# Performance work log

Measured on AMD Instinct MI355X. Metric: run time of the kernel, lower is better.

## Reference

```python
import jax, jax.numpy as jnp
import numpy as np

D = 1024      # d_model
ED = 2048     # d_inner
K = 4         # d_conv
N = 16        # d_state
R = 64        # dt_rank
E = 8         # num_experts
TOPK = 2      # num_experts_per_tok
FF = 2048     # mlp_size
EPS = 1e-6
B, L = 1, 2048


def setup_inputs() -> dict:
    key = jax.random.key(0)
    ks = jax.random.split(key, 12)
    def nrm(k, shape, scale=0.02):
        return jax.random.normal(k, shape, jnp.float32) * scale
    return {
        "x": jax.random.normal(ks[0], (B, L, D), jnp.float32),
        "rms1_w": jnp.ones((D,), jnp.float32),
        "rms2_w": jnp.ones((D,), jnp.float32),
        "W_in": nrm(ks[1], (2 * ED, D)),
        "conv_w": nrm(ks[2], (ED, 1, K), 0.1),
        "conv_b": jnp.zeros((ED,), jnp.float32),
        "W_xproj": nrm(ks[3], (R + 2 * N, ED)),
        "W_dt": nrm(ks[4], (ED, R), 0.1),
        "b_dt": jnp.full((ED,), -4.6, jnp.float32),  # softplus(-4.6) ~ 0.01 init dt
        "A_log": jnp.log(jnp.tile(jnp.arange(1, N + 1, dtype=jnp.float32), (ED, 1))),  # S4D-real init
        "D_skip": jnp.ones((ED,), jnp.float32),
        "W_out": nrm(ks[5], (D, ED)),
        "W_router": nrm(ks[6], (E, D)),
        "gate_w": nrm(ks[7], (E, FF, D)),
        "up_w": nrm(ks[8], (E, FF, D)),
        "down_w": nrm(ks[9], (E, D, FF)),
    }


def rmsnorm(x, w):
    return x * jax.lax.rsqrt(jnp.mean(x * x, -1, keepdims=True) + EPS) * w


def mamba(x, W_in, conv_w, conv_b, W_xproj, W_dt, b_dt, A_log, D_skip, W_out):
    Bb, Ll, _ = x.shape
    xm, z = jnp.split(x @ W_in.T, 2, axis=-1)                 # [B,L,ED] each
    # depthwise causal conv over time
    xc = jax.lax.conv_general_dilated(xm.transpose(0, 2, 1), conv_w, (1,), [(K - 1, 0)],
                                      feature_group_count=ED)  # [B,ED,L]
    xc = jax.nn.silu((xc + conv_b[None, :, None]).transpose(0, 2, 1))  # [B,L,ED]
    dt, Bm, Cm = jnp.split(xc @ W_xproj.T, [R, R + N], axis=-1)        # [B,L,R],[B,L,N],[B,L,N]
    delta = jax.nn.softplus(dt @ W_dt.T + b_dt)                        # [B,L,ED]
    A = -jnp.exp(A_log)                                                # [ED,N]
    dA = jnp.exp(delta[..., None] * A)                                 # [B,L,ED,N]
    dBx = delta[..., None] * Bm[:, :, None, :] * xc[..., None]         # [B,L,ED,N]

    def step(h, t):
        dA_t, dBx_t, C_t = t
        h = dA_t * h + dBx_t
        return h, jnp.einsum("ben,bn->be", h, C_t)

    h0 = jnp.zeros((Bb, ED, N), x.dtype)
    _, ys = jax.lax.scan(step, h0, (dA.transpose(1, 0, 2, 3), dBx.transpose(1, 0, 2, 3), Cm.transpose(1, 0, 2)))
    y = ys.transpose(1, 0, 2) + D_skip * xc
    y = y * jax.nn.silu(z)
    return y @ W_out.T


def moe(x2d, W_router, gate_w, up_w, down_w):
    logits = x2d @ W_router.T                                  # [T,E]
    probs = jax.nn.softmax(logits.astype(jnp.float32), -1)
    topw, sel = jax.lax.top_k(probs, TOPK)                     # NOTE: no renormalization (faithful)
    topw = topw.astype(x2d.dtype)
    wmat = jnp.sum(jax.nn.one_hot(sel, E, dtype=x2d.dtype) * topw[..., None], axis=1)  # [T,E]
    g = jnp.einsum("td,efd->tef", x2d, gate_w)
    u = jnp.einsum("td,efd->tef", x2d, up_w)
    h = jax.nn.silu(g) * u
    ye = jnp.einsum("tef,edf->ted", h, down_w)
    out = jnp.einsum("ted,te->td", ye, wmat)
    return out, logits


def reference(x, rms1_w, rms2_w, W_in, conv_w, conv_b, W_xproj, W_dt, b_dt, A_log,
              D_skip, W_out, W_router, gate_w, up_w, down_w):
    Bb, Ll, Dd = x.shape
    res = x
    h = rmsnorm(x, rms1_w)
    h = mamba(h, W_in, conv_w, conv_b, W_xproj, W_dt, b_dt, A_log, D_skip, W_out)
    x = res + h
    res = x
    h = rmsnorm(x, rms2_w)
    mo, logits = moe(h.reshape(-1, Dd), W_router, gate_w, up_w, down_w)
    x = res + mo.reshape(Bb, Ll, Dd)
    return (x, logits)
```

## Files before the change

kernel.cpp:

```cpp
#include <hip/hip_runtime.h>
#include <math.h>

typedef unsigned short u16;
typedef unsigned int   u32;
typedef __attribute__((ext_vector_type(8))) short bf16x8;
typedef __attribute__((ext_vector_type(4))) float f32x4;

constexpr int Tn=2048, Dm=1024, EDc=2048, Ns=16, Rr=64, NEx=8, FFc=2048;
constexpr int SCH=32, SNCH=Tn/SCH;
constexpr int MAXTM=40;
constexpr float LOG2E = 1.44269504f;

__device__ __forceinline__ float siluf(float x){ return __fdividef(x, 1.f + __expf(-x)); }
__device__ __forceinline__ u16 bfr(float f){
  u32 u = __float_as_uint(f);
  return (u16)((u + 0x7fffu + ((u>>16)&1u)) >> 16);
}
__device__ __forceinline__ float b2f(u16 h){ return __uint_as_float(((u32)h)<<16); }

__device__ __forceinline__ void gload16(const void* g, void* l){
  __builtin_amdgcn_global_load_lds((const __attribute__((address_space(1))) void*)g,
                                   (__attribute__((address_space(3))) void*)l, 16, 0, 0);
}

__global__ __launch_bounds__(256) void f2b_k(const float* __restrict__ in,
                                             u16* __restrict__ out, int n4){
  int i = blockIdx.x*256 + threadIdx.x;
  if (i >= n4) return;
  float4 v = ((const float4*)in)[i];
  u32 lo = (u32)bfr(v.x) | ((u32)bfr(v.y)<<16);
  u32 hi = (u32)bfr(v.z) | ((u32)bfr(v.w)<<16);
  ((uint2*)out)[i] = make_uint2(lo, hi);
}

__global__ __launch_bounds__(256) void f2b3_k(
    const float* __restrict__ g, const float* __restrict__ u,
    const float* __restrict__ d,
    u16* __restrict__ og, u16* __restrict__ ou, u16* __restrict__ od){
  const int BPW = (NEx*FFc*Dm/4)/256;
  int b = blockIdx.x;
  int which = b / BPW;
  int i = (b - which*BPW)*256 + threadIdx.x;
  const float* in = (which==0) ? g : (which==1) ? u : d;
  u16* out        = (which==0) ? og : (which==1) ? ou : od;
  float4 v = ((const float4*)in)[i];
  u32 lo = (u32)bfr(v.x) | ((u32)bfr(v.y)<<16);
  u32 hi = (u32)bfr(v.z) | ((u32)bfr(v.w)<<16);
  ((uint2*)out)[i] = make_uint2(lo, hi);
}

__global__ __launch_bounds__(256) void rmsnorm_k(const float* __restrict__ x,
                                                 const float* __restrict__ w,
                                                 u16* __restrict__ ob){
  int t = blockIdx.x;
  const float* xr = x + (size_t)t * Dm;
  float v[4]; float s = 0.f;
#pragma unroll
  for (int j = 0; j < 4; j++){ int d = threadIdx.x + j*256; v[j] = xr[d]; s += v[j]*v[j]; }
#pragma unroll
  for (int m = 1; m < 64; m <<= 1) s += __shfl_xor(s, m);
  __shared__ float red[4]; __shared__ float sb;
  int lane = threadIdx.x & 63, wv = threadIdx.x >> 6;
  if (lane == 0) red[wv] = s;
  __syncthreads();
  if (threadIdx.x == 0) sb = rsqrtf((red[0]+red[1]+red[2]+red[3]) * (1.f/Dm) + 1e-6f);
  __syncthreads();
  float sc = sb;
#pragma unroll
  for (int j = 0; j < 4; j++){
    int d = threadIdx.x + j*256;
    ob[(size_t)t*Dm + d] = bfr(v[j]*sc*w[d]);
  }
}

__global__ __launch_bounds__(256) void rms2red_k(
  const float* __restrict__ x, const float* __restrict__ P,
  const float* __restrict__ w,
  float* __restrict__ out, float* __restrict__ h2f, u16* __restrict__ h2b)
{
  int t = blockIdx.x, tid = threadIdx.x;
  const size_t S = (size_t)Tn*Dm;
  float v[4]; float s = 0.f;
#pragma unroll
  for (int j = 0; j < 4; j++){
    int d = tid + j*256;
    size_t idx = (size_t)t*Dm + d;
    float a = x[idx] + ((P[idx] + P[S+idx]) + (P[2*S+idx] + P[3*S+idx]));
    out[idx] = a; v[j] = a; s += a*a;
  }
#pragma unroll
  for (int m = 1; m < 64; m <<= 1) s += __shfl_xor(s, m);
  __shared__ float red[4]; __shared__ float sb;
  int lane = tid & 63, wv = tid >> 6;
  if (lane == 0) red[wv] = s;
  __syncthreads();
  if (tid == 0) sb = rsqrtf((red[0]+red[1]+red[2]+red[3]) * (1.f/Dm) + 1e-6f);
  __syncthreads();
  float sc = sb;
#pragma unroll
  for (int j = 0; j < 4; j++){
    int d = tid + j*256;
    float o = v[j]*sc*w[d];
    h2b[(size_t)t*Dm + d] = bfr(o);
    h2f[(size_t)t*Dm + d] = o;
  }
}

template<int EPI, int OB>
__global__ __launch_bounds__(512) void gemm_bb(
    const u16* __restrict__ A, int lda,
    const u16* __restrict__ B, int ldb,
    void* __restrict__ Cv, int ldc,
    int M, int N, int Ksl, const float* __restrict__ aux)
{
  __shared__ u16 As[2*4096], Bs[2*4096];
  int tid = threadIdx.x, lane = tid & 63, wid = tid >> 6;
  int wr = wid >> 2, wc = wid & 3;
  int n0 = blockIdx.x * 128, m0 = blockIdx.y * 128;
  int r = tid >> 2;
  int kk = ((tid & 3) ^ (r & 3)) * 8;
  size_t kbeg = (size_t)blockIdx.z * Ksl;
  const u16* Ag = A + (size_t)min(m0 + r, M-1)*lda + kbeg + kk;
  const u16* Bg = B + (size_t)min(n0 + r, N-1)*ldb + kbeg + kk;
  f32x4 acc[4][2] = {};
  int sw = ((lane>>4) ^ (lane&3)) * 8;
  int aoff[4], boff[2];
#pragma unroll
  for (int i = 0; i < 4; i++) aoff[i] = (wr*64 + i*16 + (lane&15))*32 + sw;
#pragma unroll
  for (int j = 0; j < 2; j++) boff[j] = (wc*32 + j*16 + (lane&15))*32 + sw;
  gload16(Ag, As + tid*8);
  gload16(Bg, Bs + tid*8);
  int NT = Ksl >> 5;
  for (int kt = 0; kt < NT; kt++){
    int cur = (kt & 1) * 4096;
    if (kt + 1 < NT){
      int nxt = 4096 - cur;
      gload16(Ag + (size_t)(kt+1)*32, As + nxt + tid*8);
      gload16(Bg + (size_t)(kt+1)*32, Bs + nxt + tid*8);
      asm volatile("s_waitcnt vmcnt(2)" ::: "memory");
    } else {
      asm volatile("s_waitcnt vmcnt(0)" ::: "memory");
    }
    __builtin_amdgcn_s_barrier();
    bf16x8 af[4], bv[2];
#pragma unroll
    for (int i = 0; i < 4; i++) af[i] = *(const bf16x8*)&As[cur + aoff[i]];
#pragma unroll
    for (int j = 0; j < 2; j++) bv[j] = *(const bf16x8*)&Bs[cur + boff[j]];
    asm volatile("s_waitcnt lgkmcnt(0)" ::: "memory");
    __builtin_amdgcn_sched_barrier(0);
    __builtin_amdgcn_s_barrier();
    __builtin_amdgcn_s_setprio(1);
#pragma unroll
    for (int i = 0; i < 4; i++)
#pragma unroll
      for (int j = 0; j < 2; j++)
        acc[i][j] = __builtin_amdgcn_mfma_f32_16x16x32_bf16(af[i], bv[j], acc[i][j], 0,0,0);
    __builtin_amdgcn_s_setprio(0);
  }
  float* Cf = (float*)Cv + (size_t)blockIdx.z * M * ldc;
  u16*   Cb = (u16*)Cv;
#pragma unroll
  for (int i = 0; i < 4; i++){
    int rbase = m0 + wr*64 + i*16 + ((lane>>4)<<2);
#pragma unroll
    for (int j = 0; j < 2; j++){
      int col = n0 + wc*32 + j*16 + (lane&15);
      if (col >= N) continue;
#pragma unroll
      for (int q = 0; q < 4; q++){
        int row = rbase + q;
        if (row >= M) continue;
        float v = acc[i][j][q];
        if (EPI == 1){ v += aux[col]; v = (v > 20.f) ? v : __logf(1.f + __expf(v)); }
        if (OB) Cb[(size_t)row*ldc + col] = bfr(v);
        else    Cf[(size_t)row*ldc + col] = v;
      }
    }
  }
}

__global__ __launch_bounds__(512) void gateup8(
    const u16* __restrict__ Aall,
    const u16* __restrict__ Wg, const u16* __restrict__ Wu,
    const int* __restrict__ cnt, const int* __restrict__ off,
    const int* __restrict__ bucket,
    const int* __restrict__ tmap, const int* __restrict__ ntot,
    u16* __restrict__ H)
{
  if ((int)blockIdx.y >= *ntot) return;
  int v = tmap[blockIdx.y];
  int e = v >> 16, m0 = (v & 0xFFFF) * 128;
  int Me = cnt[e];
  __shared__ u16 As[2*4096], Gs[2*4096], Us[2*4096];
  int tid = threadIdx.x, lane = tid & 63, wid = tid >> 6;
  int wr = wid >> 2, wc = wid & 3;
  int n0 = blockIdx.x * 128;
  int r = tid >> 2;
  int kk = ((tid & 3) ^ (r & 3)) * 8;
  int arow = bucket[e*Tn + min(m0 + r, Me-1)];
  const u16* Ag = Aall + (size_t)arow*Dm + kk;
  const u16* Gg = Wg + ((size_t)e*FFc + n0 + r)*Dm + kk;
  const u16* Ug = Wu + ((size_t)e*FFc + n0 + r)*Dm + kk;
  f32x4 ag[4][2] = {}, au[4][2] = {};
  int sw = ((lane>>4) ^ (lane&3)) * 8;
  int aoff[4], boff[2];
#pragma unroll
  for (int i = 0; i < 4; i++) aoff[i] = (wr*64 + i*16 + (lane&15))*32 + sw;
#pragma unroll
  for (int j = 0; j < 2; j++) boff[j] = (wc*32 + j*16 + (lane&15))*32 + sw;
  gload16(Ag, As + tid*8);
  gload16(Gg, Gs + tid*8);
  gload16(Ug, Us + tid*8);
  const int NT = Dm >> 5;
  for (int kt = 0; kt < NT; kt++){
    int cur = (kt & 1) * 4096;
    if (kt + 1 < NT){
      int nxt = 4096 - cur;
      gload16(Ag + (size_t)(kt+1)*32, As + nxt + tid*8);
      gload16(Gg + (size_t)(kt+1)*32, Gs + nxt + tid*8);
      gload16(Ug + (size_t)(kt+1)*32, Us + nxt + tid*8);
      asm volatile("s_waitcnt vmcnt(3)" ::: "memory");
    } else {
      asm volatile("s_waitcnt vmcnt(0)" ::: "memory");
    }
    __builtin_amdgcn_s_barrier();
    bf16x8 af[4], gf[2], uf[2];
#pragma unroll
    for (int i = 0; i < 4; i++) af[i] = *(const bf16x8*)&As[cur + aoff[i]];
#pragma unroll
    for (int j = 0; j < 2; j++){ gf[j] = *(const bf16x8*)&Gs[cur + boff[j]];
                                 uf[j] = *(const bf16x8*)&Us[cur + boff[j]]; }
    asm volatile("s_waitcnt lgkmcnt(0)" ::: "memory");
    __builtin_amdgcn_sched_barrier(0);
    __builtin_amdgcn_s_barrier();
    __builtin_amdgcn_s_setprio(1);
#pragma unroll
    for (int i = 0; i < 4; i++)
#pragma unroll
      for (int j = 0; j < 2; j++){
        ag[i][j] = __builtin_amdgcn_mfma_f32_16x16x32_bf16(af[i], gf[j], ag[i][j], 0,0,0);
        au[i][j] = __builtin_amdgcn_mfma_f32_16x16x32_bf16(af[i], uf[j], au[i][j], 0,0,0);
      }
    __builtin_amdgcn_s_setprio(0);
  }
  int offe = off[e];
#pragma unroll
  for (int i = 0; i < 4; i++){
    int mb = m0 + wr*64 + i*16 + ((lane>>4)<<2);
#pragma unroll
    for (int j = 0; j < 2; j++){
      int col = n0 + wc*32 + j*16 + (lane&15);
#pragma unroll
      for (int q = 0; q < 4; q++){
        int m = mb + q;
        if (m >= Me) continue;
        float g = ag[i][j][q], u = au[i][j][q];
        H[(size_t)(offe + m)*FFc + col] = bfr(siluf(g)*u);
      }
    }
  }
}

__global__ __launch_bounds__(512) void down8(
    const u16* __restrict__ Hall, const u16* __restrict__ Wd,
    const int* __restrict__ cnt, const int* __restrict__ off,
    const int* __restrict__ tmap, const int* __restrict__ ntot,
    u16* __restrict__ Y)
{
  if ((int)blockIdx.y >= *ntot) return;
  int v = tmap[blockIdx.y];
  int e = v >> 16, m0 = (v & 0xFFFF) * 128;
  int Me = cnt[e];
  int offe = off[e];
  int kbeg = blockIdx.z * (FFc/2);
  const u16* A = Hall + (size_t)offe*FFc;
  const u16* B = Wd + (size_t)e*Dm*FFc;
  u16* C = Y + (size_t)blockIdx.z*(2*Tn)*Dm + (size_t)offe*Dm;
  __shared__ u16 As[2*4096], Bs[2*4096];
  int tid = threadIdx.x, lane = tid & 63, wid = tid >> 6;
  int wr = wid >> 2, wc = wid & 3;
  int n0 = blockIdx.x * 128;
  int r = tid >> 2;
  int kk = ((tid & 3) ^ (r & 3)) * 8;
  const u16* Ag = A + (size_t)min(m0 + r, Me-1)*FFc + kbeg + kk;
  const u16* Bg = B + (size_t)(n0 + r)*FFc + kbeg + kk;
  f32x4 acc[4][2] = {};
  int sw = ((lane>>4) ^ (lane&3)) * 8;
  int aoff[4], boff[2];
#pragma unroll
  for (int i = 0; i < 4; i++) aoff[i] = (wr*64 + i*16 + (lane&15))*32 + sw;
#pragma unroll
  for (int j = 0; j < 2; j++) boff[j] = (wc*32 + j*16 + (lane&15))*32 + sw;
  gload16(Ag, As + tid*8);
  gload16(Bg, Bs + tid*8);
  const int NT = (FFc/2) >> 5;
  for (int kt = 0; kt < NT; kt++){
    int cur = (kt & 1) * 4096;
    if (kt + 1 < NT){
      int nxt = 4096 - cur;
      gload16(Ag + (size_t)(kt+1)*32, As + nxt + tid*8);
      gload16(Bg + (size_t)(kt+1)*32, Bs + nxt + tid*8);
      asm volatile("s_waitcnt vmcnt(2)" ::: "memory");
    } else {
      asm volatile("s_waitcnt vmcnt(0)" ::: "memory");
    }
    __builtin_amdgcn_s_barrier();
    bf16x8 af[4], bv[2];
#pragma unroll
    for (int i = 0; i < 4; i++) af[i] = *(const bf16x8*)&As[cur + aoff[i]];
#pragma unroll
    for (int j = 0; j < 2; j++) bv[j] = *(const bf16x8*)&Bs[cur + boff[j]];
    asm volatile("s_waitcnt lgkmcnt(0)" ::: "memory");
    __builtin_amdgcn_sched_barrier(0);
    __builtin_amdgcn_s_barrier();
    __builtin_amdgcn_s_setprio(1);
#pragma unroll
    for (int i = 0; i < 4; i++)
#pragma unroll
      for (int j = 0; j < 2; j++)
        acc[i][j] = __builtin_amdgcn_mfma_f32_16x16x32_bf16(af[i], bv[j], acc[i][j], 0,0,0);
    __builtin_amdgcn_s_setprio(0);
  }
#pragma unroll
  for (int i = 0; i < 4; i++){
    int mb = m0 + wr*64 + i*16 + ((lane>>4)<<2);
#pragma unroll
    for (int j = 0; j < 2; j++){
      int col = n0 + wc*32 + j*16 + (lane&15);
#pragma unroll
      for (int q = 0; q < 4; q++){
        int m = mb + q;
        if (m >= Me) continue;
        C[(size_t)m*Dm + col] = bfr(acc[i][j][q]);
      }
    }
  }
}

__global__ __launch_bounds__(256) void conv_k(const u16* __restrict__ xzb,
    const float* __restrict__ cw, const float* __restrict__ cb,
    u16* __restrict__ xc)
{
  int idx = blockIdx.x*256 + threadIdx.x;
  int t = idx >> 11, e = idx & (EDc - 1);
  float v = cb[e];
#pragma unroll
  for (int k = 0; k < 4; k++){
    int tt = t - 3 + k;
    if (tt >= 0) v += b2f(xzb[(size_t)tt*(2*EDc) + e]) * cw[e*4 + k];
  }
  xc[(size_t)t*EDc + e] = bfr(siluf(v));
}

__global__ __launch_bounds__(256) void xp_red(const float* __restrict__ part,
                                              float* __restrict__ xp,
                                              u16* __restrict__ dtA){
  int i = blockIdx.x*256 + threadIdx.x;
  const int S = Tn*96;
  float v = part[i] + part[S + i] + part[2*S + i] + part[3*S + i];
  xp[i] = v;
  int t = i / 96, c = i - t*96;
  if (c < Rr) dtA[t*Rr + c] = bfr(v);
}

__global__ __launch_bounds__(256) void scan_p1(
  const u16* __restrict__ delta, const u16* __restrict__ xc,
  const float* __restrict__ xp,  const float* __restrict__ A_log,
  float* __restrict__ hend, float* __restrict__ dsum)
{
  __shared__ u16 sdel[SCH*256], sxc[SCH*256];
  __shared__ float sB[SCH*16];
  int tid = threadIdx.x;
  int e0 = blockIdx.x*256, c = blockIdx.y, t0 = c*SCH;
#pragma unroll
  for (int i = 0; i < 4; i++){
    int f = (i*256+tid)*8;
    int t = f >> 8, e = f & 255;
    gload16(&delta[(size_t)(t0+t)*EDc + e0 + e], sdel + f);
    gload16(&xc  [(size_t)(t0+t)*EDc + e0 + e], sxc + f);
  }
  sB[tid]       = xp[(size_t)(t0 + (tid>>4))*96 + Rr + (tid&15)];
  sB[tid+256]   = xp[(size_t)(t0 + ((tid+256)>>4))*96 + Rr + (tid&15)];
  float a2[16];
  {
    const float* ar = &A_log[(size_t)(e0+tid)*16];
#pragma unroll
    for (int n = 0; n < 16; n++) a2[n] = -__expf(ar[n]) * LOG2E;
  }
  __syncthreads();
  float h[16] = {};
  float ds = 0.f;
  for (int t = 0; t < SCH; t++){
    float del = b2f(sdel[t*256 + tid]);
    float xv  = b2f(sxc [t*256 + tid]);
    ds += del;
    float dbx = del * xv;
    float4 b0 = *(const float4*)&sB[t*16];
    float4 b1 = *(const float4*)&sB[t*16+4];
    float4 b2 = *(const float4*)&sB[t*16+8];
    float4 b3 = *(const float4*)&sB[t*16+12];
    float bb[16] = {b0.x,b0.y,b0.z,b0.w, b1.x,b1.y,b1.z,b1.w,
                    b2.x,b2.y,b2.z,b2.w, b3.x,b3.y,b3.z,b3.w};
#pragma unroll
    for (int n = 0; n < 16; n++){
      float dA = exp2f(del * a2[n]);
      h[n] = fmaf(dA, h[n], dbx * bb[n]);
    }
  }
  float* hp = &hend[((size_t)c*EDc + e0 + tid)*16];
#pragma unroll
  for (int n = 0; n < 16; n += 4)
    *(float4*)&hp[n] = make_float4(h[n], h[n+1], h[n+2], h[n+3]);
  dsum[c*EDc + e0 + tid] = ds;
}

__global__ __launch_bounds__(256) void scan_p2(
  const float* __restrict__ hend, const float* __restrict__ dsum,
  const float* __restrict__ A_log, float* __restrict__ hin)
{
  int g = blockIdx.x*256 + threadIdx.x;
  int e = g >> 4;
  float a2 = -__expf(A_log[g]) * LOG2E;
  float h = 0.f;
  for (int c = 0; c < SNCH; c++){
    hin[(size_t)c*EDc*Ns + g] = h;
    float P = exp2f(a2 * dsum[c*EDc + e]);
    h = fmaf(P, h, hend[(size_t)c*EDc*Ns + g]);
  }
}

__global__ __launch_bounds__(256) void scan_p3(
  const u16* __restrict__ delta, const u16* __restrict__ xc,
  const float* __restrict__ xp,  const u16* __restrict__ xzb,
  const float* __restrict__ A_log, const float* __restrict__ D_skip,
  const float* __restrict__ hin,   u16* __restrict__ y2)
{
  __shared__ u16 sdel[SCH*256], sxc[SCH*256], sz[SCH*256];
  __shared__ float sB[SCH*16], sC[SCH*16];
  int tid = threadIdx.x;
  int e0 = blockIdx.x*256, c = blockIdx.y, t0 = c*SCH;
#pragma unroll
  for (int i = 0; i < 4; i++){
    int f = (i*256+tid)*8;
    int t = f >> 8, e = f & 255;
    gload16(&delta[(size_t)(t0+t)*EDc + e0 + e], sdel + f);
    gload16(&xc  [(size_t)(t0+t)*EDc + e0 + e], sxc + f);
    gload16(&xzb [(size_t)(t0+t)*(2*EDc) + EDc + e0 + e], sz + f);
  }
  {
    int f0 = tid, f1 = tid + 256;
    sB[f0] = xp[(size_t)(t0 + (f0>>4))*96 + Rr + (f0&15)];
    sB[f1] = xp[(size_t)(t0 + (f1>>4))*96 + Rr + (f1&15)];
    sC[f0] = xp[(size_t)(t0 + (f0>>4))*96 + Rr + Ns + (f0&15)];
    sC[f1] = xp[(size_t)(t0 + (f1>>4))*96 + Rr + Ns + (f1&15)];
  }
  float a2[16];
  {
    const float* ar = &A_log[(size_t)(e0+tid)*16];
#pragma unroll
    for (int n = 0; n < 16; n++) a2[n] = -__expf(ar[n]) * LOG2E;
  }
  float dsk = D_skip[e0 + tid];
  float h[16];
  {
    const float* hp = &hin[((size_t)c*EDc + e0 + tid)*16];
#pragma unroll
    for (int n = 0; n < 16; n += 4){
      float4 hv = *(const float4*)&hp[n];
      h[n] = hv.x; h[n+1] = hv.y; h[n+2] = hv.z; h[n+3] = hv.w;
    }
  }
  __syncthreads();
  for (int t = 0; t < SCH; t++){
    float del = b2f(sdel[t*256 + tid]);
    float xv  = b2f(sxc [t*256 + tid]);
    float zv  = b2f(sz  [t*256 + tid]);
    float dbx = del * xv;
    float4 b0 = *(const float4*)&sB[t*16];
    float4 b1 = *(const float4*)&sB[t*16+4];
    float4 b2 = *(const float4*)&sB[t*16+8];
    float4 b3 = *(const float4*)&sB[t*16+12];
    float bb[16] = {b0.x,b0.y,b0.z,b0.w, b1.x,b1.y,b1.z,b1.w,
                    b2.x,b2.y,b2.z,b2.w, b3.x,b3.y,b3.z,b3.w};
    float4 c0 = *(const float4*)&sC[t*16];
    float4 c1 = *(const float4*)&sC[t*16+4];
    float4 c2 = *(const float4*)&sC[t*16+8];
    float4 c3 = *(const float4*)&sC[t*16+12];
    float cc[16] = {c0.x,c0.y,c0.z,c0.w, c1.x,c1.y,c1.z,c1.w,
                    c2.x,c2.y,c2.z,c2.w, c3.x,c3.y,c3.z,c3.w};
    float p0 = 0.f, p1 = 0.f, p2 = 0.f, p3 = 0.f;
#pragma unroll
    for (int n = 0; n < 16; n += 4){
      float dA0 = exp2f(del * a2[n]);
      float dA1 = exp2f(del * a2[n+1]);
      float dA2 = exp2f(del * a2[n+2]);
      float dA3 = exp2f(del * a2[n+3]);
      h[n]   = fmaf(dA0, h[n],   dbx * bb[n]);
      h[n+1] = fmaf(dA1, h[n+1], dbx * bb[n+1]);
      h[n+2] = fmaf(dA2, h[n+2], dbx * bb[n+2]);
      h[n+3] = fmaf(dA3, h[n+3], dbx * bb[n+3]);
      p0 = fmaf(h[n],   cc[n],   p0);
      p1 = fmaf(h[n+1], cc[n+1], p1);
      p2 = fmaf(h[n+2], cc[n+2], p2);
      p3 = fmaf(h[n+3], cc[n+3], p3);
    }
    float p = (p0 + p1) + (p2 + p3);
    y2[(size_t)(t0+t)*EDc + e0 + tid] = bfr((p + dsk*xv) * siluf(zv));
  }
}

__global__ __launch_bounds__(256) void route_k(
  const float* __restrict__ h2, const float* __restrict__ Wr,
  float* __restrict__ logits_out,
  int* __restrict__ cnt, int* __restrict__ bucket,
  int* __restrict__ tok_e, int* __restrict__ tok_idx, float* __restrict__ tok_w)
{
  int t = blockIdx.x, tid = threadIdx.x;
  float p[8] = {};
#pragma unroll
  for (int j = 0; j < 4; j++){
    int d = tid + j*256;
    float xv = h2[(size_t)t*Dm + d];
#pragma unroll
    for (int e = 0; e < 8; e++) p[e] += xv * Wr[e*Dm + d];
  }
#pragma unroll
  for (int e = 0; e < 8; e++)
#pragma unroll
    for (int m = 1; m < 64; m <<= 1) p[e] += __shfl_xor(p[e], m);
  __shared__ float part[4][8];
  __shared__ float lg[8];
  int lane = tid & 63, wv = tid >> 6;
  if (lane == 0)
#pragma unroll
    for (int e = 0; e < 8; e++) part[wv][e] = p[e];
  __syncthreads();
  if (tid < 8){
    float v = part[0][tid]+part[1][tid]+part[2][tid]+part[3][tid];
    lg[tid] = v;
    logits_out[(size_t)t*8 + tid] = v;
  }
  __syncthreads();
  if (tid == 0){
    float mx = lg[0];
#pragma unroll
    for (int e = 1; e < 8; e++) mx = fmaxf(mx, lg[e]);
    float ex[8], s = 0.f;
#pragma unroll
    for (int e = 0; e < 8; e++){ ex[e] = expf(lg[e] - mx); s += ex[e]; }
    float inv = 1.f / s;
    int i0 = 0; float b0 = ex[0]*inv;
#pragma unroll
    for (int e = 1; e < 8; e++){ float pe = ex[e]*inv; if (pe > b0){ b0 = pe; i0 = e; } }
    int i1 = -1; float b1 = -1e30f;
#pragma unroll
    for (int e = 0; e < 8; e++){ if (e == i0) continue; float pe = ex[e]*inv; if (pe > b1){ b1 = pe; i1 = e; } }
    int k0 = atomicAdd(&cnt[i0], 1); bucket[i0*Tn + k0] = t;
    int k1 = atomicAdd(&cnt[i1], 1); bucket[i1*Tn + k1] = t;
    tok_e[2*t] = i0;   tok_idx[2*t] = k0;   tok_w[2*t] = b0;
    tok_e[2*t+1] = i1; tok_idx[2*t+1] = k1; tok_w[2*t+1] = b1;
  }
}

__global__ void prefix_k(const int* __restrict__ cnt, int* __restrict__ off,
                         int* __restrict__ tmap, int* __restrict__ ntot){
  if (threadIdx.x == 0 && blockIdx.x == 0){
    int s = 0;
    for (int e = 0; e < NEx; e++){ off[e] = s; s += cnt[e]; }
    int nt = 0;
    for (int e = 0; e < NEx; e++){
      int tiles = (cnt[e] + 127) >> 7;
      for (int tm = 0; tm < tiles; tm++) tmap[nt++] = (e << 16) | tm;
    }
    *ntot = nt;
  }
}

__global__ __launch_bounds__(256) void combine_k(float* __restrict__ out,
    const u16* __restrict__ Y, const int* __restrict__ off,
    const int* __restrict__ tok_e, const int* __restrict__ tok_idx,
    const float* __restrict__ tok_w)
{
  int t = blockIdx.x, tid = threadIdx.x;
  const size_t S2 = (size_t)(2*Tn)*Dm;
  int e0 = tok_e[2*t],   e1 = tok_e[2*t+1];
  size_t r0 = (size_t)(off[e0] + tok_idx[2*t])*Dm;
  size_t r1 = (size_t)(off[e1] + tok_idx[2*t+1])*Dm;
  float w0 = tok_w[2*t], w1 = tok_w[2*t+1];
#pragma unroll
  for (int j = 0; j < 4; j++){
    int d = tid + j*256;
    float y0 = b2f(Y[r0 + d]) + b2f(Y[S2 + r0 + d]);
    float y1 = b2f(Y[r1 + d]) + b2f(Y[S2 + r1 + d]);
    out[(size_t)t*Dm + d] += w0*y0 + w1*y1;
  }
}

extern "C" void kernel_launch(void* const* d_in, const int* in_sizes, int n_in,
                              void* d_out, int out_size, void* d_ws, size_t ws_size,
                              hipStream_t stream) {
  const float* x      = (const float*)d_in[0];
  const float* rms1_w = (const float*)d_in[1];
  const float* rms2_w = (const float*)d_in[2];
  const float* W_in   = (const float*)d_in[3];
  const float* conv_w = (const float*)d_in[4];
  const float* conv_b = (const float*)d_in[5];
  const float* W_xprj = (const float*)d_in[6];
  const float* W_dt   = (const float*)d_in[7];
  const float* b_dt   = (const float*)d_in[8];
  const float* A_log  = (const float*)d_in[9];
  const float* D_skip = (const float*)d_in[10];
  const float* W_out  = (const float*)d_in[11];
  const float* W_rt   = (const float*)d_in[12];
  const float* gate_w = (const float*)d_in[13];
  const float* up_w   = (const float*)d_in[14];
  const float* down_w = (const float*)d_in[15];

  float* out        = (float*)d_out;
  float* logits_out = out + (size_t)Tn*Dm;

  uint8_t* base = (uint8_t*)d_ws;
  size_t o = 0;
  auto alloc = [&](size_t bytes) -> void* {
    void* p = base + o;
    o = (o + bytes + 255) & ~(size_t)255;
    return p;
  };
  float* h2f   = (float*)alloc((size_t)Tn*Dm*4);
  u16*   h2b   = (u16*)  alloc((size_t)Tn*Dm*2);
  u16*   hmoe  = (u16*)  alloc((size_t)2*Tn*FFc*2);
  u16*   yslot = (u16*)  alloc((size_t)2*(2*Tn)*Dm*2);
  int*   cnt     = (int*)alloc(64);
  int*   off     = (int*)alloc(64);
  int*   ntot    = (int*)alloc(64);
  int*   tmap    = (int*)alloc(MAXTM*4 + 192);
  int*   bucket  = (int*)alloc((size_t)NEx*Tn*4);
  int*   tok_e   = (int*)alloc((size_t)2*Tn*4);
  int*   tok_idx = (int*)alloc((size_t)2*Tn*4);
  float* tok_w   = (float*)alloc((size_t)2*Tn*4);
  size_t oz = o;
  u16*   xzb   = (u16*)  alloc((size_t)Tn*2*EDc*2);
  u16*   delta = (u16*)  alloc((size_t)Tn*EDc*2);
  u16*   xc    = (u16*)  alloc((size_t)Tn*EDc*2);
  u16*   y2    = (u16*)  alloc((size_t)Tn*EDc*2);
  u16*   h1b   = (u16*)  alloc((size_t)Tn*Dm*2);
  u16*   dtA   = (u16*)  alloc((size_t)Tn*Rr*2);
  float* xp    = (float*)alloc((size_t)Tn*96*4);
  float* xp_part=(float*)alloc((size_t)4*Tn*96*4);
  float* hend  = (float*)alloc((size_t)SNCH*EDc*Ns*4);
  float* hin   = (float*)alloc((size_t)SNCH*EDc*Ns*4);
  float* dsum  = (float*)alloc((size_t)SNCH*EDc*4);
  float* wpart = (float*)xzb;
  u16* wgate = (u16*)(base + oz);
  u16* wup   = wgate + (size_t)NEx*FFc*Dm;
  u16* wdown = wup   + (size_t)NEx*FFc*Dm;
  u16* wbin  = (u16*)yslot;
  u16* wbout = wbin + (size_t)2*EDc*Dm;
  u16* wxp   = (u16*)hmoe;
  u16* wdt   = wxp + (size_t)96*EDc;

  f2b_k<<<(2*EDc*Dm/4)/256, 256, 0, stream>>>(W_in,   wbin,  2*EDc*Dm/4);
  f2b_k<<<(Dm*EDc/4)/256,   256, 0, stream>>>(W_out,  wbout, Dm*EDc/4);
  f2b_k<<<(96*EDc/4)/256,   256, 0, stream>>>(W_xprj, wxp,   96*EDc/4);
  f2b_k<<<(EDc*Rr/4)/256,   256, 0, stream>>>(W_dt,   wdt,   EDc*Rr/4);
  rmsnorm_k<<<Tn, 256, 0, stream>>>(x, rms1_w, h1b);
  gemm_bb<0,1><<<dim3(32,16,1), 512, 0, stream>>>(h1b, Dm, wbin, Dm, xzb, 2*EDc, Tn, 2*EDc, Dm, nullptr);
  conv_k<<<(Tn*EDc)/256, 256, 0, stream>>>(xzb, conv_w, conv_b, xc);
  gemm_bb<0,0><<<dim3(1,16,4), 512, 0, stream>>>(xc, EDc, wxp, EDc, xp_part, 96, Tn, 96, EDc/4, nullptr);
  xp_red<<<(Tn*96)/256, 256, 0, stream>>>(xp_part, xp, dtA);
  gemm_bb<1,1><<<dim3(16,16,1), 512, 0, stream>>>(dtA, Rr, wdt, Rr, delta, EDc, Tn, EDc, Rr, b_dt);
  scan_p1<<<dim3(EDc/256, SNCH), 256, 0, stream>>>(delta, xc, xp, A_log, hend, dsum);
  scan_p2<<<EDc*Ns/256, 256, 0, stream>>>(hend, dsum, A_log, hin);
  scan_p3<<<dim3(EDc/256, SNCH), 256, 0, stream>>>(delta, xc, xp, xzb, A_log, D_skip, hin, y2);
  gemm_bb<0,0><<<dim3(8,16,4), 512, 0, stream>>>(y2, EDc, wbout, EDc, wpart, Dm, Tn, Dm, EDc/4, nullptr);
  rms2red_k<<<Tn, 256, 0, stream>>>(x, wpart, rms2_w, out, h2f, h2b);
  f2b3_k<<<3*((NEx*FFc*Dm/4)/256), 256, 0, stream>>>(gate_w, up_w, down_w, wgate, wup, wdown);
  hipMemsetAsync(cnt, 0, 32, stream);
  route_k<<<Tn, 256, 0, stream>>>(h2f, W_rt, logits_out, cnt, bucket, tok_e, tok_idx, tok_w);
  prefix_k<<<1, 64, 0, stream>>>(cnt, off, tmap, ntot);
  gateup8<<<dim3(16, MAXTM), 512, 0, stream>>>(h2b, wgate, wup, cnt, off, bucket, tmap, ntot, hmoe);
  down8<<<dim3(8, MAXTM, 2), 512, 0, stream>>>(hmoe, wdown, cnt, off, tmap, ntot, yslot);
  combine_k<<<Tn, 256, 0, stream>>>(out, yslot, off, tok_e, tok_idx, tok_w);
}
```

Measured before the change: 395.7 us.

## Load MoE expert weight fragments directly into registers instead of LDS

In the gate/up and down expert GEMM kernels, the weight (B) operand tiles no longer pass through shared memory. Each lane loads its MFMA B fragments straight from global memory into registers, double-buffered one k-step ahead, and only the token activation tile is still staged in LDS. This cuts LDS traffic and footprint, which may allow more resident blocks per CU. In exchange, the global loads become less coalesced, since each lane reads 16-byte pieces from rows spaced far apart, and the weight fragments loaded by the wr=0 and wr=1 waves are fetched twice.

```diff
diff --git a/kernel.cpp b/kernel.cpp
--- a/kernel.cpp
+++ b/kernel.cpp
@@ -181,6 +181,38 @@
   }
 }
 
+#define GUP_STEP(KT, CUR, CG0,CG1,CU0,CU1, NG0,NG1,NU0,NU1)                   \
+  {                                                                           \
+    const int kt_ = (KT);                                                     \
+    const int cur_ = (CUR), nxt_ = 4096 - (CUR);                              \
+    if (kt_ + 1 < NT){                                                        \
+      gload16(Ag + (size_t)(kt_+1)*32, As + nxt_ + tid*8);                    \
+      NG0 = *(const bf16x8*)(Gf + (size_t)(kt_+1)*32);                        \
+      NG1 = *(const bf16x8*)(Gf + (size_t)(kt_+1)*32 + JS);                   \
+      NU0 = *(const bf16x8*)(Uf + (size_t)(kt_+1)*32);                        \
+      NU1 = *(const bf16x8*)(Uf + (size_t)(kt_+1)*32 + JS);                   \
+      asm volatile("s_waitcnt vmcnt(5)" ::: "memory");                        \
+    } else {                                                                  \
+      asm volatile("s_waitcnt vmcnt(0)" ::: "memory");                        \
+    }                                                                         \
+    __builtin_amdgcn_s_barrier();                                             \
+    bf16x8 af[4];                                                             \
+    _Pragma("unroll")                                                         \
+    for (int i = 0; i < 4; i++) af[i] = *(const bf16x8*)&As[cur_ + aoff[i]];  \
+    asm volatile("s_waitcnt lgkmcnt(0)" ::: "memory");                        \
+    __builtin_amdgcn_sched_barrier(0);                                        \
+    __builtin_amdgcn_s_barrier();                                             \
+    __builtin_amdgcn_s_setprio(1);                                            \
+    _Pragma("unroll")                                                         \
+    for (int i = 0; i < 4; i++){                                              \
+      ag[i][0] = __builtin_amdgcn_mfma_f32_16x16x32_bf16(af[i], CG0, ag[i][0], 0,0,0); \
+      ag[i][1] = __builtin_amdgcn_mfma_f32_16x16x32_bf16(af[i], CG1, ag[i][1], 0,0,0); \
+      au[i][0] = __builtin_amdgcn_mfma_f32_16x16x32_bf16(af[i], CU0, au[i][0], 0,0,0); \
+      au[i][1] = __builtin_amdgcn_mfma_f32_16x16x32_bf16(af[i], CU1, au[i][1], 0,0,0); \
+    }                                                                         \
+    __builtin_amdgcn_s_setprio(0);                                            \
+  }
+
 __global__ __launch_bounds__(512) void gateup8(
     const u16* __restrict__ Aall,
     const u16* __restrict__ Wg, const u16* __restrict__ Wu,
@@ -193,7 +225,7 @@
   int v = tmap[blockIdx.y];
   int e = v >> 16, m0 = (v & 0xFFFF) * 128;
   int Me = cnt[e];
-  __shared__ u16 As[2*4096], Gs[2*4096], Us[2*4096];
+  __shared__ u16 As[2*4096];
   int tid = threadIdx.x, lane = tid & 63, wid = tid >> 6;
   int wr = wid >> 2, wc = wid & 3;
   int n0 = blockIdx.x * 128;
@@ -201,49 +233,26 @@
   int kk = ((tid & 3) ^ (r & 3)) * 8;
   int arow = bucket[e*Tn + min(m0 + r, Me-1)];
   const u16* Ag = Aall + (size_t)arow*Dm + kk;
-  const u16* Gg = Wg + ((size_t)e*FFc + n0 + r)*Dm + kk;
-  const u16* Ug = Wu + ((size_t)e*FFc + n0 + r)*Dm + kk;
+  int bcol = n0 + wc*32 + (lane & 15);
+  int kfr  = (lane >> 4) * 8;
+  const u16* Gf = Wg + ((size_t)e*FFc + bcol)*Dm + kfr;
+  const u16* Uf = Wu + ((size_t)e*FFc + bcol)*Dm + kfr;
+  const size_t JS = (size_t)16 * Dm;
   f32x4 ag[4][2] = {}, au[4][2] = {};
   int sw = ((lane>>4) ^ (lane&3)) * 8;
-  int aoff[4], boff[2];
+  int aoff[4];
 #pragma unroll
   for (int i = 0; i < 4; i++) aoff[i] = (wr*64 + i*16 + (lane&15))*32 + sw;
-#pragma unroll
-  for (int j = 0; j < 2; j++) boff[j] = (wc*32 + j*16 + (lane&15))*32 + sw;
+  const int NT = Dm >> 5;
   gload16(Ag, As + tid*8);
-  gload16(Gg, Gs + tid*8);
-  gload16(Ug, Us + tid*8);
-  const int NT = Dm >> 5;
-  for (int kt = 0; kt < NT; kt++){
-    int cur = (kt & 1) * 4096;
-    if (kt + 1 < NT){
-      int nxt = 4096 - cur;
-      gload16(Ag + (size_t)(kt+1)*32, As + nxt + tid*8);
-      gload16(Gg + (size_t)(kt+1)*32, Gs + nxt + tid*8);
-      gload16(Ug + (size_t)(kt+1)*32, Us + nxt + tid*8);
-      asm volatile("s_waitcnt vmcnt(3)" ::: "memory");
-    } else {
-      asm volatile("s_waitcnt vmcnt(0)" ::: "memory");
-    }
-    __builtin_amdgcn_s_barrier();
-    bf16x8 af[4], gf[2], uf[2];
-#pragma unroll
-    for (int i = 0; i < 4; i++) af[i] = *(const bf16x8*)&As[cur + aoff[i]];
-#pragma unroll
-    for (int j = 0; j < 2; j++){ gf[j] = *(const bf16x8*)&Gs[cur + boff[j]];
-                                 uf[j] = *(const bf16x8*)&Us[cur + boff[j]]; }
-    asm volatile("s_waitcnt lgkmcnt(0)" ::: "memory");
-    __builtin_amdgcn_sched_barrier(0);
-    __builtin_amdgcn_s_barrier();
-    __builtin_amdgcn_s_setprio(1);
-#pragma unroll
-    for (int i = 0; i < 4; i++)
-#pragma unroll
-      for (int j = 0; j < 2; j++){
-        ag[i][j] = __builtin_amdgcn_mfma_f32_16x16x32_bf16(af[i], gf[j], ag[i][j], 0,0,0);
-        au[i][j] = __builtin_amdgcn_mfma_f32_16x16x32_bf16(af[i], uf[j], au[i][j], 0,0,0);
-      }
-    __builtin_amdgcn_s_setprio(0);
+  bf16x8 gA0 = *(const bf16x8*)(Gf);
+  bf16x8 gA1 = *(const bf16x8*)(Gf + JS);
+  bf16x8 uA0 = *(const bf16x8*)(Uf);
+  bf16x8 uA1 = *(const bf16x8*)(Uf + JS);
+  bf16x8 gB0 = {}, gB1 = {}, uB0 = {}, uB1 = {};
+  for (int kt = 0; kt < NT; kt += 2){
+    GUP_STEP(kt,   0,    gA0,gA1,uA0,uA1, gB0,gB1,uB0,uB1)
+    GUP_STEP(kt+1, 4096, gB0,gB1,uB0,uB1, gA0,gA1,uA0,uA1)
   }
   int offe = off[e];
 #pragma unroll
@@ -263,6 +272,34 @@
   }
 }
 
+#define DWN_STEP(KT, CUR, CB0,CB1, NB0,NB1)                                   \
+  {                                                                           \
+    const int kt_ = (KT);                                                     \
+    const int cur_ = (CUR), nxt_ = 4096 - (CUR);                              \
+    if (kt_ + 1 < NT){                                                        \
+      gload16(Ag + (size_t)(kt_+1)*32, As + nxt_ + tid*8);                    \
+      NB0 = *(const bf16x8*)(Bf + (size_t)(kt_+1)*32);                        \
+      NB1 = *(const bf16x8*)(Bf + (size_t)(kt_+1)*32 + JS);                   \
+      asm volatile("s_waitcnt vmcnt(3)" ::: "memory");                        \
+    } else {                                                                  \
+      asm volatile("s_waitcnt vmcnt(0)" ::: "memory");                        \
+    }                                                                         \
+    __builtin_amdgcn_s_barrier();                                             \
+    bf16x8 af[4];                                                             \
+    _Pragma("unroll")                                                         \
+    for (int i = 0; i < 4; i++) af[i] = *(const bf16x8*)&As[cur_ + aoff[i]];  \
+    asm volatile("s_waitcnt lgkmcnt(0)" ::: "memory");                        \
+    __builtin_amdgcn_sched_barrier(0);                                        \
+    __builtin_amdgcn_s_barrier();                                             \
+    __builtin_amdgcn_s_setprio(1);                                            \
+    _Pragma("unroll")                                                         \
+    for (int i = 0; i < 4; i++){                                              \
+      acc[i][0] = __builtin_amdgcn_mfma_f32_16x16x32_bf16(af[i], CB0, acc[i][0], 0,0,0); \
+      acc[i][1] = __builtin_amdgcn_mfma_f32_16x16x32_bf16(af[i], CB1, acc[i][1], 0,0,0); \
+    }                                                                         \
+    __builtin_amdgcn_s_setprio(0);                                            \
+  }
+
 __global__ __launch_bounds__(512) void down8(
     const u16* __restrict__ Hall, const u16* __restrict__ Wd,
     const int* __restrict__ cnt, const int* __restrict__ off,
@@ -276,52 +313,31 @@
   int offe = off[e];
   int kbeg = blockIdx.z * (FFc/2);
   const u16* A = Hall + (size_t)offe*FFc;
-  const u16* B = Wd + (size_t)e*Dm*FFc;
   u16* C = Y + (size_t)blockIdx.z*(2*Tn)*Dm + (size_t)offe*Dm;
-  __shared__ u16 As[2*4096], Bs[2*4096];
+  __shared__ u16 As[2*4096];
   int tid = threadIdx.x, lane = tid & 63, wid = tid >> 6;
   int wr = wid >> 2, wc = wid & 3;
   int n0 = blockIdx.x * 128;
   int r = tid >> 2;
   int kk = ((tid & 3) ^ (r & 3)) * 8;
   const u16* Ag = A + (size_t)min(m0 + r, Me-1)*FFc + kbeg + kk;
-  const u16* Bg = B + (size_t)(n0 + r)*FFc + kbeg + kk;
+  int bcol = n0 + wc*32 + (lane & 15);
+  int kfr  = (lane >> 4) * 8;
+  const u16* Bf = Wd + (size_t)e*Dm*FFc + (size_t)bcol*FFc + kbeg + kfr;
+  const size_t JS = (size_t)16 * FFc;
   f32x4 acc[4][2] = {};
   int sw = ((lane>>4) ^ (lane&3)) * 8;
-  int aoff[4], boff[2];
+  int aoff[4];
 #pragma unroll
   for (int i = 0; i < 4; i++) aoff[i] = (wr*64 + i*16 + (lane&15))*32 + sw;
-#pragma unroll
-  for (int j = 0; j < 2; j++) boff[j] = (wc*32 + j*16 + (lane&15))*32 + sw;
+  const int NT = (FFc/2) >> 5;
   gload16(Ag, As + tid*8);
-  gload16(Bg, Bs + tid*8);
-  const int NT = (FFc/2) >> 5;
-  for (int kt = 0; kt < NT; kt++){
-    int cur = (kt & 1) * 4096;
-    if (kt + 1 < NT){
-      int nxt = 4096 - cur;
-      gload16(Ag + (size_t)(kt+1)*32, As + nxt + tid*8);
-      gload16(Bg + (size_t)(kt+1)*32, Bs + nxt + tid*8);
-      asm volatile("s_waitcnt vmcnt(2)" ::: "memory");
-    } else {
-      asm volatile("s_waitcnt vmcnt(0)" ::: "memory");
-    }
-    __builtin_amdgcn_s_barrier();
-    bf16x8 af[4], bv[2];
-#pragma unroll
-    for (int i = 0; i < 4; i++) af[i] = *(const bf16x8*)&As[cur + aoff[i]];
-#pragma unroll
-    for (int j = 0; j < 2; j++) bv[j] = *(const bf16x8*)&Bs[cur + boff[j]];
-    asm volatile("s_waitcnt lgkmcnt(0)" ::: "memory");
-    __builtin_amdgcn_sched_barrier(0);
-    __builtin_amdgcn_s_barrier();
-    __builtin_amdgcn_s_setprio(1);
-#pragma unroll
-    for (int i = 0; i < 4; i++)
-#pragma unroll
-      for (int j = 0; j < 2; j++)
-        acc[i][j] = __builtin_amdgcn_mfma_f32_16x16x32_bf16(af[i], bv[j], acc[i][j], 0,0,0);
-    __builtin_amdgcn_s_setprio(0);
+  bf16x8 bA0 = *(const bf16x8*)(Bf);
+  bf16x8 bA1 = *(const bf16x8*)(Bf + JS);
+  bf16x8 bB0 = {}, bB1 = {};
+  for (int kt = 0; kt < NT; kt += 2){
+    DWN_STEP(kt,   0,    bA0,bA1, bB0,bB1)
+    DWN_STEP(kt+1, 4096, bB0,bB1, bA0,bA1)
   }
 #pragma unroll
   for (int i = 0; i < 4; i++){
```

Result: slower. 451.7 us (+14.2%).

## Reshape MoE gate/up tile to 256 tokens by 64 FF columns

Applied to the files above, without the earlier changes.

The gate/up grouped GEMM now uses 256-row token tiles and 64-column FF tiles instead of 128x128. Each weight tile row is then loaded once per 256 tokens, and half the threads fetch gate while the other half fetch up. A separate 256-row tile map is built for gate/up, and the down projection keeps its 128-row map. This cuts weight traffic, which dominates the expert GEMM, but it pads more rows for experts with few tokens and the 8 waves are now arranged 4x2.

```diff
diff --git a/kernel.cpp b/kernel.cpp
--- a/kernel.cpp
+++ b/kernel.cpp
@@ -9,6 +9,7 @@
 constexpr int Tn=2048, Dm=1024, EDc=2048, Ns=16, Rr=64, NEx=8, FFc=2048;
 constexpr int SCH=32, SNCH=Tn/SCH;
 constexpr int MAXTM=40;
+constexpr int MAXTM2=24;
 constexpr float LOG2E = 1.44269504f;
 
 __device__ __forceinline__ float siluf(float x){ return __fdividef(x, 1.f + __expf(-x)); }
@@ -191,18 +192,22 @@
 {
   if ((int)blockIdx.y >= *ntot) return;
   int v = tmap[blockIdx.y];
-  int e = v >> 16, m0 = (v & 0xFFFF) * 128;
+  int e = v >> 16, m0 = (v & 0xFFFF) * 256;
   int Me = cnt[e];
-  __shared__ u16 As[2*4096], Gs[2*4096], Us[2*4096];
+  __shared__ u16 As[2*8192], Gs[2*2048], Us[2*2048];
   int tid = threadIdx.x, lane = tid & 63, wid = tid >> 6;
-  int wr = wid >> 2, wc = wid & 3;
-  int n0 = blockIdx.x * 128;
+  int wr = wid >> 1, wc = wid & 1;
+  int n0 = blockIdx.x * 64;
   int r = tid >> 2;
   int kk = ((tid & 3) ^ (r & 3)) * 8;
-  int arow = bucket[e*Tn + min(m0 + r, Me-1)];
-  const u16* Ag = Aall + (size_t)arow*Dm + kk;
-  const u16* Gg = Wg + ((size_t)e*FFc + n0 + r)*Dm + kk;
-  const u16* Ug = Wu + ((size_t)e*FFc + n0 + r)*Dm + kk;
+  int arow  = bucket[e*Tn + min(m0 + r,       Me-1)];
+  int arow2 = bucket[e*Tn + min(m0 + 128 + r, Me-1)];
+  const u16* Ag  = Aall + (size_t)arow *Dm + kk;
+  const u16* Ag2 = Aall + (size_t)arow2*Dm + kk;
+  int rg = r & 63;
+  const u16* GUg = ((tid < 256) ? Wg : Wu) + ((size_t)e*FFc + n0 + rg)*Dm + kk;
+  u16* GUsb = (tid < 256) ? (u16*)Gs : (u16*)Us;
+  int g8 = (tid & 255) * 8;
   f32x4 ag[4][2] = {}, au[4][2] = {};
   int sw = ((lane>>4) ^ (lane&3)) * 8;
   int aoff[4], boff[2];
@@ -210,17 +215,17 @@
   for (int i = 0; i < 4; i++) aoff[i] = (wr*64 + i*16 + (lane&15))*32 + sw;
 #pragma unroll
   for (int j = 0; j < 2; j++) boff[j] = (wc*32 + j*16 + (lane&15))*32 + sw;
-  gload16(Ag, As + tid*8);
-  gload16(Gg, Gs + tid*8);
-  gload16(Ug, Us + tid*8);
   const int NT = Dm >> 5;
+  gload16(Ag,  As + tid*8);
+  gload16(Ag2, As + 4096 + tid*8);
+  gload16(GUg, GUsb + g8);
   for (int kt = 0; kt < NT; kt++){
-    int cur = (kt & 1) * 4096;
+    int cab = (kt & 1) * 8192, cgu = (kt & 1) * 2048;
     if (kt + 1 < NT){
-      int nxt = 4096 - cur;
-      gload16(Ag + (size_t)(kt+1)*32, As + nxt + tid*8);
-      gload16(Gg + (size_t)(kt+1)*32, Gs + nxt + tid*8);
-      gload16(Ug + (size_t)(kt+1)*32, Us + nxt + tid*8);
+      int nab = 8192 - cab, ngu = 2048 - cgu;
+      gload16(Ag  + (size_t)(kt+1)*32, As + nab + tid*8);
+      gload16(Ag2 + (size_t)(kt+1)*32, As + nab + 4096 + tid*8);
+      gload16(GUg + (size_t)(kt+1)*32, GUsb + ngu + g8);
       asm volatile("s_waitcnt vmcnt(3)" ::: "memory");
     } else {
       asm volatile("s_waitcnt vmcnt(0)" ::: "memory");
@@ -228,10 +233,10 @@
     __builtin_amdgcn_s_barrier();
     bf16x8 af[4], gf[2], uf[2];
 #pragma unroll
-    for (int i = 0; i < 4; i++) af[i] = *(const bf16x8*)&As[cur + aoff[i]];
-#pragma unroll
-    for (int j = 0; j < 2; j++){ gf[j] = *(const bf16x8*)&Gs[cur + boff[j]];
-                                 uf[j] = *(const bf16x8*)&Us[cur + boff[j]]; }
+    for (int i = 0; i < 4; i++) af[i] = *(const bf16x8*)&As[cab + aoff[i]];
+#pragma unroll
+    for (int j = 0; j < 2; j++){ gf[j] = *(const bf16x8*)&Gs[cgu + boff[j]];
+                                 uf[j] = *(const bf16x8*)&Us[cgu + boff[j]]; }
     asm volatile("s_waitcnt lgkmcnt(0)" ::: "memory");
     __builtin_amdgcn_sched_barrier(0);
     __builtin_amdgcn_s_barrier();
@@ -266,11 +271,11 @@
 __global__ __launch_bounds__(512) void down8(
     const u16* __restrict__ Hall, const u16* __restrict__ Wd,
     const int* __restrict__ cnt, const int* __restrict__ off,
-    const int* __restrict__ tmap, const int* __restrict__ ntot,
+    const int* __restrict__ tmap2, const int* __restrict__ ntot2,
     u16* __restrict__ Y)
 {
-  if ((int)blockIdx.y >= *ntot) return;
-  int v = tmap[blockIdx.y];
+  if ((int)blockIdx.y >= *ntot2) return;
+  int v = tmap2[blockIdx.y];
   int e = v >> 16, m0 = (v & 0xFFFF) * 128;
   int Me = cnt[e];
   int offe = off[e];
@@ -565,16 +570,23 @@
 }
 
 __global__ void prefix_k(const int* __restrict__ cnt, int* __restrict__ off,
-                         int* __restrict__ tmap, int* __restrict__ ntot){
+                         int* __restrict__ tmap, int* __restrict__ ntot,
+                         int* __restrict__ tmap2, int* __restrict__ ntot2){
   if (threadIdx.x == 0 && blockIdx.x == 0){
     int s = 0;
     for (int e = 0; e < NEx; e++){ off[e] = s; s += cnt[e]; }
     int nt = 0;
     for (int e = 0; e < NEx; e++){
+      int tiles = (cnt[e] + 255) >> 8;
+      for (int tm = 0; tm < tiles; tm++) tmap[nt++] = (e << 16) | tm;
+    }
+    *ntot = nt;
+    int n2 = 0;
+    for (int e = 0; e < NEx; e++){
       int tiles = (cnt[e] + 127) >> 7;
-      for (int tm = 0; tm < tiles; tm++) tmap[nt++] = (e << 16) | tm;
-    }
-    *ntot = nt;
+      for (int tm = 0; tm < tiles; tm++) tmap2[n2++] = (e << 16) | tm;
+    }
+    *ntot2 = n2;
   }
 }
 
@@ -635,7 +647,9 @@
   int*   cnt     = (int*)alloc(64);
   int*   off     = (int*)alloc(64);
   int*   ntot    = (int*)alloc(64);
-  int*   tmap    = (int*)alloc(MAXTM*4 + 192);
+  int*   ntot2   = (int*)alloc(64);
+  int*   tmap    = (int*)alloc(MAXTM2*4 + 192);
+  int*   tmap2   = (int*)alloc(MAXTM*4 + 192);
   int*   bucket  = (int*)alloc((size_t)NEx*Tn*4);
   int*   tok_e   = (int*)alloc((size_t)2*Tn*4);
   int*   tok_idx = (int*)alloc((size_t)2*Tn*4);
@@ -679,8 +693,8 @@
   f2b3_k<<<3*((NEx*FFc*Dm/4)/256), 256, 0, stream>>>(gate_w, up_w, down_w, wgate, wup, wdown);
   hipMemsetAsync(cnt, 0, 32, stream);
   route_k<<<Tn, 256, 0, stream>>>(h2f, W_rt, logits_out, cnt, bucket, tok_e, tok_idx, tok_w);
-  prefix_k<<<1, 64, 0, stream>>>(cnt, off, tmap, ntot);
-  gateup8<<<dim3(16, MAXTM), 512, 0, stream>>>(h2b, wgate, wup, cnt, off, bucket, tmap, ntot, hmoe);
-  down8<<<dim3(8, MAXTM, 2), 512, 0, stream>>>(hmoe, wdown, cnt, off, tmap, ntot, yslot);
+  prefix_k<<<1, 64, 0, stream>>>(cnt, off, tmap, ntot, tmap2, ntot2);
+  gateup8<<<dim3(32, MAXTM2), 512, 0, stream>>>(h2b, wgate, wup, cnt, off, bucket, tmap, ntot, hmoe);
+  down8<<<dim3(8, MAXTM, 2), 512, 0, stream>>>(hmoe, wdown, cnt, off, tmap2, ntot2, yslot);
   combine_k<<<Tn, 256, 0, stream>>>(out, yslot, off, tok_e, tok_idx, tok_w);
 }
```

Result: no change. 397.2 us (+0.4%).
